# Kernel optimization log

Measured on AMD Instinct MI355X. Metric: run time of the kernel, lower is better.

The kernel has to match this reference:

```python
import jax, jax.numpy as jnp
import numpy as np

D = 1024
HEAD_DIM = D // 16  # attention_heads=16, used only for the softmax scale


def setup_inputs() -> dict:
    key = jax.random.key(0)
    ks = jax.random.split(key, 9)
    s = 1.0 / np.sqrt(D)
    return {
        "features": jax.random.normal(ks[0], (4, 2048, D), dtype=jnp.float32),
        "Wq": jax.random.normal(ks[1], (D, D), dtype=jnp.float32) * s,
        "bq": jnp.zeros((D,), dtype=jnp.float32),
        "Wk": jax.random.normal(ks[2], (D, D), dtype=jnp.float32) * s,
        "bk": jnp.zeros((D,), dtype=jnp.float32),
        "Wv": jax.random.normal(ks[3], (D, D), dtype=jnp.float32) * s,
        "bv": jnp.zeros((D,), dtype=jnp.float32),
        "Wo": jax.random.normal(ks[4], (D, D), dtype=jnp.float32) * s,
        "bo": jnp.zeros((D,), dtype=jnp.float32),
    }


def reference(features, Wq, bq, Wk, bk, Wv, bv, Wo, bo):
    # torch nn.Linear: x @ W.T + b
    q = features @ Wq.T + bq  # [B, S, D]
    k = features @ Wk.T + bk
    v = features @ Wv.T + bv
    scale = 1.0 / np.sqrt(HEAD_DIM).astype(np.float32)
    scores = jnp.einsum("bsd,btd->bst", q, k) * scale  # [B, S, S]
    weights = jax.nn.softmax(scores, axis=-1)
    out = jnp.einsum("bst,btd->bsd", weights, v)
    return out @ Wo.T + bo
```

## Files before the change

kernel.cpp:

```cpp
#include <hip/hip_runtime.h>


using u16 = unsigned short;
typedef __bf16 bf16x8 __attribute__((ext_vector_type(8)));
typedef float f32x4 __attribute__((ext_vector_type(4)));

#define AS1 __attribute__((address_space(1)))
#define AS3 __attribute__((address_space(3)))

__device__ inline u16 f2bf(float f) {
  union { float f; unsigned int u; } c; c.f = f;
  unsigned int u = c.u;
  u += 0x7fffu + ((u >> 16) & 1u);
  return (u16)(u >> 16);
}

__global__ __launch_bounds__(256) void cast_all(
    const float4* __restrict__ feat, const float4* __restrict__ wq,
    const float4* __restrict__ wk, const float4* __restrict__ wv,
    const float4* __restrict__ wo, ushort4* __restrict__ xbf,
    ushort4* __restrict__ wcat, float* __restrict__ lsum) {
  const int b = blockIdx.x, tx = threadIdx.x;
  if (b >= 12288) {
    lsum[(b - 12288) * 256 + tx] = 0.f;
    return;
  }
  const float4* src; ushort4* dst; int idx;
  if (b < 8192) { src = feat; dst = xbf; idx = b * 256 + tx; }
  else {
    const int w = (b - 8192) >> 10, loc = ((b - 8192) & 1023) * 256 + tx;
    src = (w == 0) ? wq : (w == 1) ? wk : (w == 2) ? wv : wo;
    dst = wcat + w * 262144; idx = loc;
  }
  float4 v = src[idx];
  ushort4 o;
  o.x = f2bf(v.x); o.y = f2bf(v.y); o.z = f2bf(v.z); o.w = f2bf(v.w);
  dst[idx] = o;
}

template <int MODE>
__global__ __launch_bounds__(256) void gemm_bt(
    const u16* __restrict__ A, const u16* __restrict__ Bm, void* __restrict__ C,
    void* __restrict__ C2, void* __restrict__ C3,
    const float* __restrict__ bias, const float* __restrict__ bias2,
    const float* __restrict__ bias3, float* __restrict__ lsum,
    int M, int N, int K, int lda, int ldc,
    float scale,
    long long sA, long long sB, long long sC)
{
  __shared__ u16 As[128 * 64];
  __shared__ u16 Bs[128 * 64];
  const int tx = threadIdx.x;
  const int wave = tx >> 6, lane = tx & 63;
  const int wm = (wave >> 1) * 64, wn = (wave & 1) * 64;

  const int nwg = gridDim.x * gridDim.y * gridDim.z;
  const int f = blockIdx.x + gridDim.x * (blockIdx.y + gridDim.y * blockIdx.z);
  const int w = (f & 7) * (nwg >> 3) + (f >> 3);
  const int bx = w % gridDim.x;
  const int rem = w / gridDim.x;
  const int by = rem % gridDim.y;
  const int bz = rem / gridDim.y;

  const int m0 = by * 128, n0 = bx * 128;
  const u16* Ab = A + bz * sA + (long long)m0 * lda;
  const u16* Bb = Bm + bz * sB + (long long)n0 * K;

  f32x4 acc[4][4] = {};

  int rT[4], qT[4];
#pragma unroll
  for (int t = 0; t < 4; ++t) {
    rT[t] = t * 32 + wave * 8 + (lane >> 3);
    qT[t] = (((lane & 7) - rT[t]) & 7) << 3;
  }
  const int ldsT[4] = {wave * 512, 2048 + wave * 512, 4096 + wave * 512,
                       6144 + wave * 512};

  const int fr = lane & 15, fq = lane >> 4;

  for (int k0 = 0; k0 < K; k0 += 64) {
#pragma unroll
    for (int t = 0; t < 4; ++t) {
      __builtin_amdgcn_global_load_lds(
          (const AS1 void*)(Ab + (long long)rT[t] * lda + k0 + qT[t]),
          (AS3 void*)(As + ldsT[t]), 16, 0, 0);
      __builtin_amdgcn_global_load_lds(
          (const AS1 void*)(Bb + (long long)rT[t] * K + k0 + qT[t]),
          (AS3 void*)(Bs + ldsT[t]), 16, 0, 0);
    }
    __syncthreads();

#pragma unroll
    for (int s = 0; s < 2; ++s) {
      bf16x8 af[4], bfv[4];
#pragma unroll
      for (int i = 0; i < 4; ++i) {
        const int Ra = wm + i * 16 + fr;
        const int Rb = wn + i * 16 + fr;
        af[i]  = *(const bf16x8*)(As + Ra * 64 + (((s * 4 + fq + Ra) & 7) << 3));
        bfv[i] = *(const bf16x8*)(Bs + Rb * 64 + (((s * 4 + fq + Rb) & 7) << 3));
      }
#pragma unroll
      for (int i = 0; i < 4; ++i)
#pragma unroll
        for (int j = 0; j < 4; ++j)
          acc[i][j] = __builtin_amdgcn_mfma_f32_16x16x32_bf16(af[i], bfv[j], acc[i][j], 0, 0, 0);
    }
    __syncthreads();
  }

  const int col = lane & 15, rq = (lane >> 4) << 2;
  const long long zC = (long long)bz * sC;

  if constexpr (MODE == 5) {
    float rsum[4][4] = {};
#pragma unroll
    for (int i = 0; i < 4; ++i) {
#pragma unroll
      for (int j = 0; j < 4; ++j) {
        const int gn = n0 + wn + j * 16 + col;
#pragma unroll
        for (int r = 0; r < 4; ++r) {
          const int gm = m0 + wm + i * 16 + rq + r;
          const float e = __expf(acc[i][j][r] * scale);
          ((u16*)C)[zC + (long long)gm * ldc + gn] = f2bf(e);
          rsum[i][r] += e;
        }
      }
    }
#pragma unroll
    for (int i = 0; i < 4; ++i) {
#pragma unroll
      for (int r = 0; r < 4; ++r) {
        float s = rsum[i][r];
        s += __shfl_xor(s, 1); s += __shfl_xor(s, 2);
        s += __shfl_xor(s, 4); s += __shfl_xor(s, 8);
        if (col == 0)
          atomicAdd(&lsum[(long long)bz * 2048 + m0 + wm + i * 16 + rq + r], s);
      }
    }
  } else if constexpr (MODE == 4) {
    float inv[4][4];
#pragma unroll
    for (int i = 0; i < 4; ++i)
#pragma unroll
      for (int r = 0; r < 4; ++r)
        inv[i][r] = 1.0f / lsum[(long long)bz * 2048 + m0 + wm + i * 16 + rq + r];
#pragma unroll
    for (int i = 0; i < 4; ++i)
#pragma unroll
      for (int j = 0; j < 4; ++j) {
        const int gn = n0 + wn + j * 16 + col;
#pragma unroll
        for (int r = 0; r < 4; ++r) {
          const int gm = m0 + wm + i * 16 + rq + r;
          ((u16*)C)[zC + (long long)gm * ldc + gn] = f2bf(acc[i][j][r] * inv[i][r]);
        }
      }
  } else if constexpr (MODE == 3) {
    const int sect = n0 >> 10;
#pragma unroll
    for (int i = 0; i < 4; ++i) {
#pragma unroll
      for (int j = 0; j < 4; ++j) {
        const int gn = n0 + wn + j * 16 + col;
        const int nb = gn & 1023;
        const float bv = (sect == 0) ? bias[nb] : (sect == 1) ? bias2[nb] : bias3[nb];
#pragma unroll
        for (int r = 0; r < 4; ++r) {
          const int gm = m0 + wm + i * 16 + rq + r;
          const float v = acc[i][j][r] + bv;
          if (sect == 0) {
            ((u16*)C)[(long long)gm * 1024 + nb] = f2bf(v);
          } else if (sect == 1) {
            ((u16*)C2)[(long long)gm * 1024 + nb] = f2bf(v);
          } else {
            const int bb = gm >> 11, t = gm & 2047;
            ((u16*)C3)[((long long)bb << 21) + (long long)nb * 2048 + t] = f2bf(v);
          }
        }
      }
    }
  } else {
#pragma unroll
    for (int i = 0; i < 4; ++i) {
#pragma unroll
      for (int j = 0; j < 4; ++j) {
        const int gn = n0 + wn + j * 16 + col;
        const float bv = bias[gn];
#pragma unroll
        for (int r = 0; r < 4; ++r) {
          const int gm = m0 + wm + i * 16 + rq + r;
          ((float*)C)[zC + (long long)gm * ldc + gn] = acc[i][j][r] + bv;
        }
      }
    }
  }
}

extern "C" void kernel_launch(void* const* d_in, const int* in_sizes, int n_in,
                              void* d_out, int out_size, void* d_ws, size_t ws_size,
                              hipStream_t stream) {
  (void)in_sizes; (void)n_in; (void)out_size; (void)ws_size;
  const float* feat = (const float*)d_in[0];
  const float* Wq = (const float*)d_in[1];
  const float* bq = (const float*)d_in[2];
  const float* Wk = (const float*)d_in[3];
  const float* bk = (const float*)d_in[4];
  const float* Wv = (const float*)d_in[5];
  const float* bv = (const float*)d_in[6];
  const float* Wo = (const float*)d_in[7];
  const float* bo = (const float*)d_in[8];
  float* out = (float*)d_out;

  char* ws = (char*)d_ws;
  const unsigned long long MB = 1024ull * 1024ull;
  u16* Xbf  = (u16*)(ws);
  u16* Wcat = (u16*)(ws + 16 * MB);
  u16* Wob  = Wcat + 3ll * 1024 * 1024;
  u16* Q    = (u16*)(ws + 24 * MB);
  u16* Kbuf = (u16*)(ws + 40 * MB);
  u16* Vt   = (u16*)(ws + 56 * MB);
  u16* P    = (u16*)(ws + 72 * MB);
  float* lsum = (float*)(ws + 104 * MB);
  u16* attn = Q;

  dim3 blk(256);

  cast_all<<<12320, blk, 0, stream>>>((const float4*)feat, (const float4*)Wq,
                                      (const float4*)Wk, (const float4*)Wv,
                                      (const float4*)Wo, (ushort4*)Xbf,
                                      (ushort4*)Wcat, lsum);

  gemm_bt<3><<<dim3(24, 64, 1), blk, 0, stream>>>(
      Xbf, Wcat, Q, Kbuf, Vt, bq, bk, bv, nullptr,
      8192, 3072, 1024, 1024, 0, 1.f, 0, 0, 0);

  gemm_bt<5><<<dim3(16, 16, 4), blk, 0, stream>>>(
      Q, Kbuf, P, nullptr, nullptr, nullptr, nullptr, nullptr, lsum,
      2048, 2048, 1024, 1024, 2048, 0.125f,
      2048ll * 1024, 2048ll * 1024, 2048ll * 2048);

  gemm_bt<4><<<dim3(8, 16, 4), blk, 0, stream>>>(
      P, Vt, attn, nullptr, nullptr, nullptr, nullptr, nullptr, lsum,
      2048, 1024, 2048, 2048, 1024, 1.f,
      2048ll * 2048, 1024ll * 2048, 2048ll * 1024);

  gemm_bt<2><<<dim3(8, 64, 1), blk, 0, stream>>>(
      attn, Wob, out, nullptr, nullptr, bo, nullptr, nullptr, nullptr,
      8192, 1024, 1024, 1024, 1024, 1.f, 0, 0, 0);
}
```

Baseline: 309.7 us.

## Load B operand directly from global into registers with double-buffered prefetch

Drops the LDS tile for the B operand. Each wave now loads its B fragments straight from global memory into registers, double-buffered so the next k-slice's B loads are issued before the current MFMA block runs. A still goes through LDS via global_load_lds. This cuts LDS traffic and shared memory per block, but B is no longer shared between the two waves that cover the same columns, so global/L2 reads of B double and register pressure rises.

```diff
diff --git a/kernel.cpp b/kernel.cpp
--- a/kernel.cpp
+++ b/kernel.cpp
@@ -49,7 +49,6 @@
     long long sA, long long sB, long long sC)
 {
   __shared__ u16 As[128 * 64];
-  __shared__ u16 Bs[128 * 64];
   const int tx = threadIdx.x;
   const int wave = tx >> 6, lane = tx & 63;
   const int wm = (wave >> 1) * 64, wn = (wave & 1) * 64;
@@ -79,34 +78,52 @@
 
   const int fr = lane & 15, fq = lane >> 4;
 
-  for (int k0 = 0; k0 < K; k0 += 64) {
-#pragma unroll
-    for (int t = 0; t < 4; ++t) {
+  auto stageA = [&](int k0) {
+#pragma unroll
+    for (int t = 0; t < 4; ++t)
       __builtin_amdgcn_global_load_lds(
           (const AS1 void*)(Ab + (long long)rT[t] * lda + k0 + qT[t]),
           (AS3 void*)(As + ldsT[t]), 16, 0, 0);
-      __builtin_amdgcn_global_load_lds(
-          (const AS1 void*)(Bb + (long long)rT[t] * K + k0 + qT[t]),
-          (AS3 void*)(Bs + ldsT[t]), 16, 0, 0);
-    }
-    __syncthreads();
-
+  };
+  auto loadB = [&](int k0, bf16x8 (&bv)[4][2]) {
+#pragma unroll
+    for (int j = 0; j < 4; ++j) {
+      const u16* Brow = Bb + (long long)(wn + j * 16 + fr) * K + k0 + fq * 8;
+#pragma unroll
+      for (int s = 0; s < 2; ++s)
+        bv[j][s] = *(const bf16x8*)(Brow + s * 32);
+    }
+  };
+  auto compute = [&](const bf16x8 (&bv)[4][2]) {
 #pragma unroll
     for (int s = 0; s < 2; ++s) {
-      bf16x8 af[4], bfv[4];
+      bf16x8 af[4];
 #pragma unroll
       for (int i = 0; i < 4; ++i) {
         const int Ra = wm + i * 16 + fr;
-        const int Rb = wn + i * 16 + fr;
-        af[i]  = *(const bf16x8*)(As + Ra * 64 + (((s * 4 + fq + Ra) & 7) << 3));
-        bfv[i] = *(const bf16x8*)(Bs + Rb * 64 + (((s * 4 + fq + Rb) & 7) << 3));
+        af[i] = *(const bf16x8*)(As + Ra * 64 + (((s * 4 + fq + Ra) & 7) << 3));
       }
 #pragma unroll
       for (int i = 0; i < 4; ++i)
 #pragma unroll
         for (int j = 0; j < 4; ++j)
-          acc[i][j] = __builtin_amdgcn_mfma_f32_16x16x32_bf16(af[i], bfv[j], acc[i][j], 0, 0, 0);
-    }
+          acc[i][j] = __builtin_amdgcn_mfma_f32_16x16x32_bf16(af[i], bv[j][s], acc[i][j], 0, 0, 0);
+    }
+  };
+
+  bf16x8 bvA[4][2], bvB[4][2];
+  loadB(0, bvA);
+  for (int k0 = 0; k0 < K; k0 += 128) {
+    stageA(k0);
+    __syncthreads();
+    loadB(k0 + 64, bvB);
+    compute(bvA);
+    __syncthreads();
+
+    stageA(k0 + 64);
+    __syncthreads();
+    if (k0 + 128 < K) loadB(k0 + 128, bvA);
+    compute(bvB);
     __syncthreads();
   }
 
```

Result: slower. 435.5 us (+40.6%).
